# Kernel tuning notes

Hardware: AMD Instinct MI355X
Metric: run time of the kernel (lower is better)

The kernel has to match this reference:

```python
import jax, jax.numpy as jnp
import numpy as np

B, N, K, C_IN, C_OUT = 8, 24576, 16, 64, 64
BN_EPS = 1e-5


def setup_inputs() -> dict:
    key = jax.random.key(0)
    k1, k2, k3, k4, k5 = jax.random.split(key, 5)
    x = jax.random.normal(k1, (B, N, C_IN), dtype=jnp.float32)
    W = jax.random.normal(k2, (C_OUT, C_IN), dtype=jnp.float32) * 0.05  # Linear weight (no bias)
    # BN affine params; module inits gamma to `init` (0.0) but that zeroes the output,
    # so we use a perturbed gamma for a meaningful correctness baseline.
    gamma = 1.0 + 0.1 * jax.random.normal(k3, (C_OUT,), dtype=jnp.float32)
    beta = 0.1 * jax.random.normal(k4, (C_OUT,), dtype=jnp.float32)
    knn = jax.random.randint(k5, (B, N, K), 0, N, dtype=jnp.int32)
    return {"x": x, "W": W, "gamma": gamma, "beta": beta, "knn": knn}


def _vector_feature(h, knn):
    # h: [B, N, C], knn: [B, N, K] -> max over neighbors of (h_j - h_i): [B, N, C]
    b, n, k = knn.shape
    nbr = jnp.take_along_axis(h, knn.reshape(b, n * k, 1), axis=1).reshape(b, n, k, -1)
    return jnp.max(nbr - h[:, :, None, :], axis=2)


def reference(x, W, gamma, beta, knn):
    h = jnp.einsum('bnc,oc->bno', x, W)            # linear, no bias
    v = _vector_feature(h, knn)                    # knn edge max-pool
    # BatchNorm1d in training mode: batch stats over B*N rows, per channel
    mean = jnp.mean(v, axis=(0, 1))
    var = jnp.mean(jnp.square(v - mean), axis=(0, 1))  # biased variance
    out = (v - mean) * jax.lax.rsqrt(var + BN_EPS) * gamma + beta
    return out
```

## Files before the change

### kernel.cpp

```cpp
#include <hip/hip_runtime.h>
#include <hip/hip_bf16.h>

typedef short s16x8 __attribute__((ext_vector_type(8)));
typedef float f32x4 __attribute__((ext_vector_type(4)));
typedef unsigned short u16x8 __attribute__((ext_vector_type(8)));

static constexpr int Bc   = 8;
static constexpr int Nn   = 24576;
static constexpr int Kk   = 16;
static constexpr int Cc   = 64;
static constexpr int Rr   = Bc * Nn;
static constexpr float EPS = 1e-5f;

__device__ __forceinline__ unsigned short f2bf(float f) {
    union { float f; unsigned int u; } c; c.f = f;
    unsigned int r = c.u + 0x7FFFu + ((c.u >> 16) & 1u);
    return (unsigned short)(r >> 16);
}
__device__ __forceinline__ float bf2f(unsigned short u) {
    union { unsigned int u; float f; } c; c.u = ((unsigned int)u) << 16; return c.f;
}
__device__ __forceinline__ float bflo(unsigned g) {
    union { unsigned u; float f; } c; c.u = g << 16; return c.f;
}
__device__ __forceinline__ float bfhi(unsigned g) {
    union { unsigned u; float f; } c; c.u = g & 0xffff0000u; return c.f;
}
__device__ __forceinline__ unsigned packbf(float lo, float hi) {
    return (unsigned)f2bf(lo) | ((unsigned)f2bf(hi) << 16);
}

__global__ __launch_bounds__(256) void linear_mfma_kernel(
    const float* __restrict__ x, const float* __restrict__ W,
    __hip_bfloat16* __restrict__ h, float* __restrict__ stats)
{
    if (blockIdx.x == 0 && threadIdx.x < 128) stats[threadIdx.x] = 0.f;

    const int tid  = threadIdx.x;
    const int l    = tid & 63;
    const int wave = tid >> 6;
    const int batch = blockIdx.x & 7;
    const int qb    = blockIdx.x >> 3;
    const int wib   = qb * 4 + wave;

    const int lr = l & 15;
    const int kg = (l >> 4) * 8;
    const int dr = (l >> 4) * 4;

    s16x8 bfrag[4][2];
#pragma unroll
    for (int ct = 0; ct < 4; ++ct)
#pragma unroll
        for (int kc = 0; kc < 2; ++kc) {
            const float* bp = W + (ct * 16 + lr) * 64 + kc * 32 + kg;
            f32x4 b0 = *reinterpret_cast<const f32x4*>(bp);
            f32x4 b1 = *reinterpret_cast<const f32x4*>(bp + 4);
            s16x8 f;
            f[0] = (short)f2bf(b0[0]); f[1] = (short)f2bf(b0[1]);
            f[2] = (short)f2bf(b0[2]); f[3] = (short)f2bf(b0[3]);
            f[4] = (short)f2bf(b1[0]); f[5] = (short)f2bf(b1[1]);
            f[6] = (short)f2bf(b1[2]); f[7] = (short)f2bf(b1[3]);
            bfrag[ct][kc] = f;
        }

    unsigned short* hu = (unsigned short*)h;
    const int tiles_per_batch = Nn / 16;
    for (int t = wib; t < tiles_per_batch; t += 1024) {
        const int row0 = batch * Nn + t * 16;
        const float* ap = x + (size_t)(row0 + lr) * 64 + kg;
        f32x4 a0 = *reinterpret_cast<const f32x4*>(ap);
        f32x4 a1 = *reinterpret_cast<const f32x4*>(ap + 4);
        f32x4 a2 = *reinterpret_cast<const f32x4*>(ap + 32);
        f32x4 a3 = *reinterpret_cast<const f32x4*>(ap + 36);
        s16x8 fa0, fa1;
        fa0[0] = (short)f2bf(a0[0]); fa0[1] = (short)f2bf(a0[1]);
        fa0[2] = (short)f2bf(a0[2]); fa0[3] = (short)f2bf(a0[3]);
        fa0[4] = (short)f2bf(a1[0]); fa0[5] = (short)f2bf(a1[1]);
        fa0[6] = (short)f2bf(a1[2]); fa0[7] = (short)f2bf(a1[3]);
        fa1[0] = (short)f2bf(a2[0]); fa1[1] = (short)f2bf(a2[1]);
        fa1[2] = (short)f2bf(a2[2]); fa1[3] = (short)f2bf(a2[3]);
        fa1[4] = (short)f2bf(a3[0]); fa1[5] = (short)f2bf(a3[1]);
        fa1[6] = (short)f2bf(a3[2]); fa1[7] = (short)f2bf(a3[3]);

        f32x4 acc[4];
#pragma unroll
        for (int ct = 0; ct < 4; ++ct) { acc[ct] = (f32x4){0.f, 0.f, 0.f, 0.f}; }
#pragma unroll
        for (int ct = 0; ct < 4; ++ct) {
            acc[ct] = __builtin_amdgcn_mfma_f32_16x16x32_bf16(fa0, bfrag[ct][0], acc[ct], 0, 0, 0);
            acc[ct] = __builtin_amdgcn_mfma_f32_16x16x32_bf16(fa1, bfrag[ct][1], acc[ct], 0, 0, 0);
        }
#pragma unroll
        for (int ct = 0; ct < 4; ++ct)
#pragma unroll
            for (int r = 0; r < 4; ++r)
                hu[(size_t)(row0 + dr + r) * 64 + ct * 16 + lr] = f2bf(acc[ct][r]);
    }
}

__global__ __launch_bounds__(256) void gather_bn_kernel(
    const __hip_bfloat16* __restrict__ h, const int* __restrict__ knn,
    __hip_bfloat16* __restrict__ v, float* __restrict__ stats)
{
    const int tid   = threadIdx.x;
    const int l     = tid & 63;
    const int wave  = tid >> 6;
    const int batch = blockIdx.x & 7;
    const int qb    = blockIdx.x >> 3;
    const int wib   = qb * 4 + wave;

    const unsigned* hu32 = (const unsigned*)h;
    unsigned* vu32 = (unsigned*)v;
    const int bbase = batch * Nn;

    const int half = l >> 5;
    const int c2   = l & 31;
    const int kl   = l & 15;

    float sum_lo = 0.f, sum_hi = 0.f, sq_lo = 0.f, sq_hi = 0.f;

    for (int r = wib * 4; r < Nn; r += 4096) {
        const int rowA = bbase + r + half;
        const int rowC = bbase + r + 2 + half;
        const int ia = knn[(size_t)rowA * Kk + kl];
        const int ic = knn[(size_t)rowC * Kk + kl];
        const unsigned oa = hu32[(size_t)rowA * 32 + c2];
        const unsigned oc = hu32[(size_t)rowC * 32 + c2];
        float mAlo = -3e38f, mAhi = -3e38f, mClo = -3e38f, mChi = -3e38f;
#pragma unroll
        for (int k = 0; k < Kk; ++k) {
            const int ja = __shfl(ia, (l & 32) + k);
            const int jc = __shfl(ic, (l & 32) + k);
            const unsigned ga = hu32[(size_t)(bbase + ja) * 32 + c2];
            const unsigned gc = hu32[(size_t)(bbase + jc) * 32 + c2];
            mAlo = fmaxf(mAlo, bflo(ga)); mAhi = fmaxf(mAhi, bfhi(ga));
            mClo = fmaxf(mClo, bflo(gc)); mChi = fmaxf(mChi, bfhi(gc));
        }
        const float vAlo = mAlo - bflo(oa), vAhi = mAhi - bfhi(oa);
        const float vClo = mClo - bflo(oc), vChi = mChi - bfhi(oc);
        vu32[(size_t)rowA * 32 + c2] = packbf(vAlo, vAhi);
        vu32[(size_t)rowC * 32 + c2] = packbf(vClo, vChi);
        sum_lo += vAlo + vClo; sum_hi += vAhi + vChi;
        sq_lo  += vAlo * vAlo + vClo * vClo;
        sq_hi  += vAhi * vAhi + vChi * vChi;
    }

    sum_lo += __shfl_xor(sum_lo, 32); sum_hi += __shfl_xor(sum_hi, 32);
    sq_lo  += __shfl_xor(sq_lo, 32);  sq_hi  += __shfl_xor(sq_hi, 32);

    __shared__ float s[4][4][32];
    if (half == 0) {
        s[0][wave][c2] = sum_lo; s[1][wave][c2] = sum_hi;
        s[2][wave][c2] = sq_lo;  s[3][wave][c2] = sq_hi;
    }
    __syncthreads();
    if (wave == 0 && half == 0) {
        const float a0 = s[0][0][c2] + s[0][1][c2] + s[0][2][c2] + s[0][3][c2];
        const float a1 = s[1][0][c2] + s[1][1][c2] + s[1][2][c2] + s[1][3][c2];
        const float q0 = s[2][0][c2] + s[2][1][c2] + s[2][2][c2] + s[2][3][c2];
        const float q1 = s[3][0][c2] + s[3][1][c2] + s[3][2][c2] + s[3][3][c2];
        atomicAdd(&stats[2 * c2],      a0);
        atomicAdd(&stats[2 * c2 + 1],  a1);
        atomicAdd(&stats[64 + 2 * c2], q0);
        atomicAdd(&stats[64 + 2 * c2 + 1], q1);
    }
}

__global__ __launch_bounds__(256) void norm_kernel(
    const __hip_bfloat16* __restrict__ v, const float* __restrict__ stats,
    const float* __restrict__ gamma, const float* __restrict__ beta,
    float* __restrict__ out)
{
    __shared__ float sc[64], sh[64];
    if (threadIdx.x < 64) {
        const int o = threadIdx.x;
        const float inv = 1.0f / (float)Rr;
        const float mean = stats[o] * inv;
        const float var  = stats[64 + o] * inv - mean * mean;
        const float s    = gamma[o] * rsqrtf(var + EPS);
        sc[o] = s;
        sh[o] = beta[o] - mean * s;
    }
    __syncthreads();

    const int batch = blockIdx.x & 7;
    const int qb    = blockIdx.x >> 3;
    const u16x8* vu = (const u16x8*)v;
    const int per_batch8 = Nn * 64 / 8;
    const size_t base8 = (size_t)batch * per_batch8;

    for (int li = qb * 256 + threadIdx.x; li < per_batch8; li += 256 * 256) {
        const size_t i = base8 + li;
        u16x8 t = vu[i];
        const int c = (li * 8) & 63;
        f32x4 r0, r1;
        r0[0] = bf2f(t[0]) * sc[c + 0] + sh[c + 0];
        r0[1] = bf2f(t[1]) * sc[c + 1] + sh[c + 1];
        r0[2] = bf2f(t[2]) * sc[c + 2] + sh[c + 2];
        r0[3] = bf2f(t[3]) * sc[c + 3] + sh[c + 3];
        r1[0] = bf2f(t[4]) * sc[c + 4] + sh[c + 4];
        r1[1] = bf2f(t[5]) * sc[c + 5] + sh[c + 5];
        r1[2] = bf2f(t[6]) * sc[c + 6] + sh[c + 6];
        r1[3] = bf2f(t[7]) * sc[c + 7] + sh[c + 7];
        f32x4* op = reinterpret_cast<f32x4*>(out + i * 8);
        __builtin_nontemporal_store(r0, op);
        __builtin_nontemporal_store(r1, op + 1);
    }
}

extern "C" void kernel_launch(void* const* d_in, const int* in_sizes, int n_in,
                              void* d_out, int out_size, void* d_ws, size_t ws_size,
                              hipStream_t stream)
{
    const float* x     = (const float*)d_in[0];
    const float* W     = (const float*)d_in[1];
    const float* gamma = (const float*)d_in[2];
    const float* beta  = (const float*)d_in[3];
    const int*   knn   = (const int*)d_in[4];
    float*       out   = (float*)d_out;

    __hip_bfloat16* h = (__hip_bfloat16*)d_ws;
    __hip_bfloat16* v = h + (size_t)Rr * 64;
    float* stats = (float*)((char*)d_ws + 2 * (size_t)Rr * 64 * sizeof(__hip_bfloat16));

    linear_mfma_kernel<<<2048, 256, 0, stream>>>(x, W, h, stats);
    gather_bn_kernel<<<2048, 256, 0, stream>>>(h, knn, v, stats);
    norm_kernel<<<2048, 256, 0, stream>>>(v, stats, gamma, beta, out);
}
```

Measured before the change: 253.6 us.

## Widen gather loads to 8 bytes per lane and process 8 rows per wave iteration

The gather/max kernel is remapped so each lane covers 4 channels with 8-byte loads, and 16 lanes cover one 128-byte row. Each wave now handles 8 rows per iteration over a fixed 3-iteration loop of 24 contiguous rows. Neighbor indices are broadcast with readlane plus selects instead of shuffles. The aim is fewer memory and shuffle instructions and more independent gathers in flight, at the cost of more scalar readlanes and a hard-coded row partition tied to the grid size.

```diff
diff --git a/kernel.cpp b/kernel.cpp
--- a/kernel.cpp
+++ b/kernel.cpp
@@ -4,6 +4,7 @@
 typedef short s16x8 __attribute__((ext_vector_type(8)));
 typedef float f32x4 __attribute__((ext_vector_type(4)));
 typedef unsigned short u16x8 __attribute__((ext_vector_type(8)));
+typedef unsigned int u32x2 __attribute__((ext_vector_type(2)));
 
 static constexpr int Bc   = 8;
 static constexpr int Nn   = 24576;
@@ -103,7 +104,7 @@
     __hip_bfloat16* __restrict__ v, float* __restrict__ stats)
 {
     const int tid   = threadIdx.x;
-    const int l     = tid & 63;
+    const int lane  = tid & 63;
     const int wave  = tid >> 6;
     const int batch = blockIdx.x & 7;
     const int qb    = blockIdx.x >> 3;
@@ -113,56 +114,88 @@
     unsigned* vu32 = (unsigned*)v;
     const int bbase = batch * Nn;
 
-    const int half = l >> 5;
-    const int c2   = l & 31;
-    const int kl   = l & 15;
-
-    float sum_lo = 0.f, sum_hi = 0.f, sq_lo = 0.f, sq_hi = 0.f;
-
-    for (int r = wib * 4; r < Nn; r += 4096) {
-        const int rowA = bbase + r + half;
-        const int rowC = bbase + r + 2 + half;
-        const int ia = knn[(size_t)rowA * Kk + kl];
-        const int ic = knn[(size_t)rowC * Kk + kl];
-        const unsigned oa = hu32[(size_t)rowA * 32 + c2];
-        const unsigned oc = hu32[(size_t)rowC * 32 + c2];
-        float mAlo = -3e38f, mAhi = -3e38f, mClo = -3e38f, mChi = -3e38f;
+    const int g  = lane >> 4;
+    const int cl = lane & 15;
+    const int c0 = cl * 4;
+
+    float sum[4] = {0.f, 0.f, 0.f, 0.f};
+    float sq[4]  = {0.f, 0.f, 0.f, 0.f};
+
+    const int rbase = bbase + wib * 24;
+#pragma unroll 1
+    for (int it = 0; it < 3; ++it) {
+        const int r0 = rbase + it * 8;
+        const int iA = knn[(size_t)r0 * Kk + lane];
+        const int iB = knn[(size_t)r0 * Kk + 64 + lane];
+        const u32x2 oA = *reinterpret_cast<const u32x2*>(hu32 + (size_t)r0 * 32 + lane * 2);
+        const u32x2 oB = *reinterpret_cast<const u32x2*>(hu32 + (size_t)r0 * 32 + 128 + lane * 2);
+
+        float mA0 = -3e38f, mA1 = -3e38f, mA2 = -3e38f, mA3 = -3e38f;
+        float mB0 = -3e38f, mB1 = -3e38f, mB2 = -3e38f, mB3 = -3e38f;
 #pragma unroll
         for (int k = 0; k < Kk; ++k) {
-            const int ja = __shfl(ia, (l & 32) + k);
-            const int jc = __shfl(ic, (l & 32) + k);
-            const unsigned ga = hu32[(size_t)(bbase + ja) * 32 + c2];
-            const unsigned gc = hu32[(size_t)(bbase + jc) * 32 + c2];
-            mAlo = fmaxf(mAlo, bflo(ga)); mAhi = fmaxf(mAhi, bfhi(ga));
-            mClo = fmaxf(mClo, bflo(gc)); mChi = fmaxf(mChi, bfhi(gc));
-        }
-        const float vAlo = mAlo - bflo(oa), vAhi = mAhi - bfhi(oa);
-        const float vClo = mClo - bflo(oc), vChi = mChi - bfhi(oc);
-        vu32[(size_t)rowA * 32 + c2] = packbf(vAlo, vAhi);
-        vu32[(size_t)rowC * 32 + c2] = packbf(vClo, vChi);
-        sum_lo += vAlo + vClo; sum_hi += vAhi + vChi;
-        sq_lo  += vAlo * vAlo + vClo * vClo;
-        sq_hi  += vAhi * vAhi + vChi * vChi;
-    }
-
-    sum_lo += __shfl_xor(sum_lo, 32); sum_hi += __shfl_xor(sum_hi, 32);
-    sq_lo  += __shfl_xor(sq_lo, 32);  sq_hi  += __shfl_xor(sq_hi, 32);
-
-    __shared__ float s[4][4][32];
-    if (half == 0) {
-        s[0][wave][c2] = sum_lo; s[1][wave][c2] = sum_hi;
-        s[2][wave][c2] = sq_lo;  s[3][wave][c2] = sq_hi;
+            const int a0 = __builtin_amdgcn_readlane(iA, k);
+            const int a1 = __builtin_amdgcn_readlane(iA, 16 + k);
+            const int a2 = __builtin_amdgcn_readlane(iA, 32 + k);
+            const int a3 = __builtin_amdgcn_readlane(iA, 48 + k);
+            const int b0 = __builtin_amdgcn_readlane(iB, k);
+            const int b1 = __builtin_amdgcn_readlane(iB, 16 + k);
+            const int b2 = __builtin_amdgcn_readlane(iB, 32 + k);
+            const int b3 = __builtin_amdgcn_readlane(iB, 48 + k);
+            const int tA0 = (g & 1) ? a1 : a0;
+            const int tA1 = (g & 1) ? a3 : a2;
+            const int jA  = (g & 2) ? tA1 : tA0;
+            const int tB0 = (g & 1) ? b1 : b0;
+            const int tB1 = (g & 1) ? b3 : b2;
+            const int jB  = (g & 2) ? tB1 : tB0;
+            const u32x2 ga = *reinterpret_cast<const u32x2*>(hu32 + (size_t)(bbase + jA) * 32 + cl * 2);
+            const u32x2 gb = *reinterpret_cast<const u32x2*>(hu32 + (size_t)(bbase + jB) * 32 + cl * 2);
+            mA0 = fmaxf(mA0, bflo(ga[0])); mA1 = fmaxf(mA1, bfhi(ga[0]));
+            mA2 = fmaxf(mA2, bflo(ga[1])); mA3 = fmaxf(mA3, bfhi(ga[1]));
+            mB0 = fmaxf(mB0, bflo(gb[0])); mB1 = fmaxf(mB1, bfhi(gb[0]));
+            mB2 = fmaxf(mB2, bflo(gb[1])); mB3 = fmaxf(mB3, bfhi(gb[1]));
+        }
+        const float vA0 = mA0 - bflo(oA[0]);
+        const float vA1 = mA1 - bfhi(oA[0]);
+        const float vA2 = mA2 - bflo(oA[1]);
+        const float vA3 = mA3 - bfhi(oA[1]);
+        const float vB0 = mB0 - bflo(oB[0]);
+        const float vB1 = mB1 - bfhi(oB[0]);
+        const float vB2 = mB2 - bflo(oB[1]);
+        const float vB3 = mB3 - bfhi(oB[1]);
+
+        u32x2 sA, sB;
+        sA[0] = packbf(vA0, vA1); sA[1] = packbf(vA2, vA3);
+        sB[0] = packbf(vB0, vB1); sB[1] = packbf(vB2, vB3);
+        *reinterpret_cast<u32x2*>(vu32 + (size_t)r0 * 32 + lane * 2) = sA;
+        *reinterpret_cast<u32x2*>(vu32 + (size_t)r0 * 32 + 128 + lane * 2) = sB;
+
+        sum[0] += vA0 + vB0; sum[1] += vA1 + vB1;
+        sum[2] += vA2 + vB2; sum[3] += vA3 + vB3;
+        sq[0]  += vA0 * vA0 + vB0 * vB0; sq[1] += vA1 * vA1 + vB1 * vB1;
+        sq[2]  += vA2 * vA2 + vB2 * vB2; sq[3] += vA3 * vA3 + vB3 * vB3;
+    }
+
+    float st[8] = {sum[0], sum[1], sum[2], sum[3], sq[0], sq[1], sq[2], sq[3]};
+#pragma unroll
+    for (int j = 0; j < 8; ++j) {
+        st[j] += __shfl_xor(st[j], 16);
+        st[j] += __shfl_xor(st[j], 32);
+    }
+
+    __shared__ float sred[4][16][8];
+    if (g == 0) {
+#pragma unroll
+        for (int j = 0; j < 8; ++j) sred[wave][cl][j] = st[j];
     }
     __syncthreads();
-    if (wave == 0 && half == 0) {
-        const float a0 = s[0][0][c2] + s[0][1][c2] + s[0][2][c2] + s[0][3][c2];
-        const float a1 = s[1][0][c2] + s[1][1][c2] + s[1][2][c2] + s[1][3][c2];
-        const float q0 = s[2][0][c2] + s[2][1][c2] + s[2][2][c2] + s[2][3][c2];
-        const float q1 = s[3][0][c2] + s[3][1][c2] + s[3][2][c2] + s[3][3][c2];
-        atomicAdd(&stats[2 * c2],      a0);
-        atomicAdd(&stats[2 * c2 + 1],  a1);
-        atomicAdd(&stats[64 + 2 * c2], q0);
-        atomicAdd(&stats[64 + 2 * c2 + 1], q1);
+    if (wave == 0 && g == 0) {
+#pragma unroll
+        for (int j = 0; j < 8; ++j) {
+            const float t = sred[0][cl][j] + sred[1][cl][j] + sred[2][cl][j] + sred[3][cl][j];
+            if (j < 4) atomicAdd(&stats[c0 + j], t);
+            else       atomicAdd(&stats[64 + c0 + (j - 4)], t);
+        }
     }
 }
 
```

Measured after the change: 348.8 us. 37.6% more time.
